# Optimization experiments

Hardware: AMD Instinct MI355X
Metric: run time of the kernel (lower is better)

Reference implementation:

```python
import jax, jax.numpy as jnp
import numpy as np

B, N, K, D, H, L = 2, 2048, 256, 768, 150, 11
REL_PROP = 2
NB = 10  # distance buckets


def _lin(key, din, dout):
    return jax.random.normal(key, (din, dout), dtype=jnp.float32) / np.sqrt(din)


def setup_inputs() -> dict:
    key = jax.random.key(0)
    ks = jax.random.split(key, 16)
    rng = np.random.default_rng(0)
    prune_idx = jnp.asarray(np.stack([np.sort(rng.permutation(N)[:K]) for _ in range(B)]), dtype=jnp.int32)
    span_begin = jnp.sort(jax.random.randint(ks[2], (B, K), 0, N - 16), axis=-1).astype(jnp.int32)
    span_end = (span_begin + jax.random.randint(ks[3], (B, K), 1, 16)).astype(jnp.int32)
    return {
        "all_span_vecs": jax.random.normal(ks[0], (B, N, D), dtype=jnp.float32),
        "update": jax.random.normal(ks[1], (B, K, D), dtype=jnp.float32),
        "square_mask": jnp.ones((B, K, K), dtype=jnp.float32),
        "span_lengths": jnp.full((B,), float(K), dtype=jnp.float32),
        "span_begin": span_begin,
        "span_end": span_end,
        "prune_indices": prune_idx,
        "w_left": _lin(ks[4], D, H), "b_left": jnp.zeros((H,), jnp.float32),
        "w_right": _lin(ks[5], D, H), "b_right": jnp.zeros((H,), jnp.float32),
        "dist_emb": jax.random.normal(ks[6], (NB, H), dtype=jnp.float32) * 0.02,
        "w_h": _lin(ks[7], H, H), "b_h": jnp.zeros((H,), jnp.float32),
        "w_out": _lin(ks[8], H, L), "b_out": jnp.zeros((L,), jnp.float32),
        "a_w": _lin(ks[9], L, D),
        "gate_w": _lin(ks[10], 2 * D, D), "gate_b": jnp.zeros((D,), jnp.float32),
        "pr_w": _lin(ks[11], D, 1), "pr_b": jnp.zeros((1,), jnp.float32),
    }


def _pair_scores(u, bins, w_left, b_left, w_right, b_right, dist_emb, w_h, b_h, w_out, b_out):
    # OptFFpairs: left/right span projections + pairwise distance embedding -> FF -> L labels
    left = u @ w_left + b_left          # [B,K,H]
    right = u @ w_right + b_right       # [B,K,H]
    h = jax.nn.relu(left[:, :, None, :] + right[:, None, :, :] + dist_emb[bins])  # [B,K,K,H]
    h = jax.nn.relu(h @ w_h + b_h)
    return h @ w_out + b_out            # [B,K,K,L]


def _add_unary(rel, ss):
    # relation_add_scores: add per-span pruner scores along both pair axes; ss: [B,K,1]
    return rel + ss[:, :, None, :] + ss[:, None, :, :]


def reference(all_span_vecs, update, square_mask, span_lengths, span_begin, span_end,
              prune_indices, w_left, b_left, w_right, b_right, dist_emb, w_h, b_h,
              w_out, b_out, a_w, gate_w, gate_b, pr_w, pr_b):
    bins = jnp.clip(jnp.abs(span_begin[:, None, :] - span_begin[:, :, None]), 0, NB - 1)  # [B,K,K]
    rel = _pair_scores(update, bins, w_left, b_left, w_right, b_right, dist_emb, w_h, b_h, w_out, b_out)
    rel = _add_unary(rel, update @ pr_w + pr_b)
    for _ in range(REL_PROP):
        probs = jax.nn.relu(rel) * square_mask[..., None]     # [B,K,K,L]
        msg = probs @ a_w                                     # A(probs): [B,K,K,D]
        # ctxt[b,j,d] = sum_i msg[b,i,j,d] * update[b,i,d] / span_lengths[b]
        ctxt = (msg * update[:, :, None, :]).sum(-3) / span_lengths[:, None, None]
        g = jax.nn.sigmoid(jnp.concatenate([update, ctxt], axis=-1) @ gate_w + gate_b)
        update = g * update + (1.0 - g) * ctxt                # MyGate
        rel = _pair_scores(update, bins, w_left, b_left, w_right, b_right, dist_emb, w_h, b_h, w_out, b_out)
        rel = _add_unary(rel, update @ pr_w + pr_b)           # pruner.scorer(update)
    # overwrite_spans: scatter updated filtered spans back into the full span tensor
    valid = jnp.arange(K)[None, :] < span_lengths[:, None]    # [B,K]
    bidx = jnp.arange(B)[:, None]
    orig = all_span_vecs[bidx, prune_indices]                 # [B,K,D]
    vals = jnp.where(valid[..., None], update, orig)
    update_all = all_span_vecs.at[bidx, prune_indices].set(vals)
    return update_all, update, rel
```

## Files before the change

kernel.cpp:

```cpp
#include <hip/hip_runtime.h>
#include <hip/hip_bf16.h>
#include <math.h>

#define BB 2
#define NN 2048
#define KK 256
#define DD 768
#define HH 150
#define LL 11
#define NBINS 10

#define KP 160
#define WP 40
#define GWP 136
#define BPAD 264

typedef __attribute__((ext_vector_type(8))) short short8;
typedef __attribute__((ext_vector_type(4))) short s16x4;
typedef __attribute__((ext_vector_type(4))) float f32x4;

#define AS_GLOBAL const __attribute__((address_space(1))) void*
#define AS_LDS __attribute__((address_space(3))) void*

__device__ inline unsigned bf2u(float lo, float hi) {
  union { __hip_bfloat162 b; unsigned u; } cv;
  cv.b = __float22bfloat162_rn(make_float2(lo, hi));
  return cv.u;
}
__device__ inline short bf1(float x) {
  union { __hip_bfloat16 b; short s; } cv;
  cv.b = __float2bfloat16(x);
  return cv.s;
}
__device__ inline float ubf(short b) {
  return __uint_as_float(((unsigned)(unsigned short)b) << 16);
}

#define PRE_PREP 110
#define PRE_CVT  192
#define PRE_TRGW 1152
#define PRE_TRWLR 240
#define PRE_TRUPD 384
#define PRE_NB (PRE_PREP + PRE_CVT + PRE_TRGW + PRE_TRWLR + PRE_TRUPD)

__global__ __launch_bounds__(256) void k_pre(
    const float* __restrict__ w_h, const float* __restrict__ w_out,
    short* __restrict__ wt, short* __restrict__ wo,
    const float* __restrict__ upd_in, short* __restrict__ updbf,
    const float* __restrict__ gate_w, short* __restrict__ gwt,
    const float* __restrict__ w_left, const float* __restrict__ w_right,
    short* __restrict__ wlrt, short* __restrict__ updT)
{
  __shared__ float tile[32][33];
  int bid = blockIdx.x;
  int t = threadIdx.x;

  if (bid < PRE_PREP) {
    int idx = bid * 256 + t;
    if (idx < KP * KP) {
      int n = idx / KP, k = idx - n * KP;
      float v = (n < HH && k < HH) ? w_h[k * HH + n] : 0.f;
      wt[idx] = bf1(v);
    }
    int idx2 = idx - KP * KP;
    if (idx2 >= 0 && idx2 < 16 * KP) {
      int n = idx2 / KP, k = idx2 - n * KP;
      float v = (n < LL && k < HH) ? w_out[k * LL + n] : 0.f;
      wo[idx2] = bf1(v);
    }
    return;
  }
  bid -= PRE_PREP;
  if (bid < PRE_CVT) {
    int idx = (bid * 256 + t) * 8;
    const float4* s4 = (const float4*)(upd_in + idx);
    float4 a = s4[0], c = s4[1];
    int4 pk;
    pk.x = (int)bf2u(a.x, a.y);
    pk.y = (int)bf2u(a.z, a.w);
    pk.z = (int)bf2u(c.x, c.y);
    pk.w = (int)bf2u(c.z, c.w);
    *(int4*)(updbf + idx) = pk;
    return;
  }
  bid -= PRE_CVT;
  if (bid < PRE_TRGW) {
    int kt = bid % 48, nt = bid / 48;
    int m0 = kt * 32, n0 = nt * 32;
    int tx = t & 31, ty = t >> 5;
    #pragma unroll
    for (int r = 0; r < 4; ++r)
      tile[ty + r * 8][tx] = gate_w[(size_t)(m0 + ty + r * 8) * DD + n0 + tx];
    __syncthreads();
    #pragma unroll
    for (int r = 0; r < 4; ++r)
      gwt[(size_t)(n0 + ty + r * 8) * (2 * DD) + m0 + tx] = bf1(tile[tx][ty + r * 8]);
    return;
  }
  bid -= PRE_TRGW;
  if (bid < PRE_TRWLR) {
    int kt = bid % 24, nt = bid / 24;
    int k0 = kt * 32, n0 = nt * 32;
    const float* src = (n0 >= KP) ? w_right : w_left;
    int col0 = n0 - (n0 >= KP ? KP : 0);
    int tx = t & 31, ty = t >> 5;
    #pragma unroll
    for (int r = 0; r < 4; ++r) {
      int col = col0 + tx;
      tile[ty + r * 8][tx] = (col < HH) ? src[(size_t)(k0 + ty + r * 8) * HH + col] : 0.f;
    }
    __syncthreads();
    #pragma unroll
    for (int r = 0; r < 4; ++r)
      wlrt[(size_t)(n0 + ty + r * 8) * DD + k0 + tx] = bf1(tile[tx][ty + r * 8]);
    return;
  }
  bid -= PRE_TRWLR;
  {
    int b = bid / 192;
    int r = bid - b * 192;
    int it = r & 7, dt = r >> 3;
    int i0 = it * 32, d0 = dt * 32;
    int tx = t & 31, ty = t >> 5;
    #pragma unroll
    for (int rr = 0; rr < 4; ++rr)
      tile[ty + rr * 8][tx] = upd_in[(size_t)(b * KK + i0 + ty + rr * 8) * DD + d0 + tx];
    __syncthreads();
    #pragma unroll
    for (int rr = 0; rr < 4; ++rr)
      updT[(size_t)(b * DD + d0 + ty + rr * 8) * KK + i0 + tx] = bf1(tile[tx][ty + rr * 8]);
  }
}

__global__ __launch_bounds__(256) void k_projss(
    const short* __restrict__ updbf, const short* __restrict__ wlrt,
    const float* __restrict__ b_left, const float* __restrict__ b_right,
    const float* __restrict__ updf, const float* __restrict__ pr_w,
    const float* __restrict__ pr_b,
    float* __restrict__ left, float* __restrict__ right, float* __restrict__ ssv)
{
  __shared__ short As[64][WP];
  __shared__ short Bs[KP][WP];
  int bidx = blockIdx.x;
  int t = threadIdx.x;

  if (bidx >= 16) {
    int row = (bidx - 16) * 4 + (t >> 6);
    int l = t & 63;
    float s = 0.f;
    for (int d = l; d < DD; d += 64) s = fmaf(updf[(size_t)row * DD + d], pr_w[d], s);
    #pragma unroll
    for (int off = 32; off > 0; off >>= 1) s += __shfl_down(s, off);
    if (l == 0) ssv[row] = s + pr_b[0];
    return;
  }

  int rbk = bidx >> 1, half = bidx & 1;
  int row0 = rbk * 64;
  const short* wsrc = wlrt + (size_t)half * KP * DD;
  int l = t & 63, w = t >> 6, lr = l & 15, lg = l >> 4;
  int ar = t >> 2, ac = t & 3;
  int i1 = t + 256, i2 = t + 512;
  f32x4 acc[10];
  #pragma unroll
  for (int nt = 0; nt < 10; ++nt) acc[nt] = (f32x4){0.f, 0.f, 0.f, 0.f};

  short8 pa, pb0, pb1, pb2 = {};
  pa  = *(const short8*)(updbf + (size_t)(row0 + ar) * DD + ac * 8);
  pb0 = *(const short8*)(wsrc + (size_t)(t >> 2) * DD + (t & 3) * 8);
  pb1 = *(const short8*)(wsrc + (size_t)(i1 >> 2) * DD + (i1 & 3) * 8);
  if (i2 < 640) pb2 = *(const short8*)(wsrc + (size_t)(i2 >> 2) * DD + (i2 & 3) * 8);

  for (int ks = 0; ks < 24; ++ks) {
    __syncthreads();
    *(short8*)&As[ar][ac * 8] = pa;
    *(short8*)&Bs[t >> 2][(t & 3) * 8] = pb0;
    *(short8*)&Bs[i1 >> 2][(i1 & 3) * 8] = pb1;
    if (i2 < 640) *(short8*)&Bs[i2 >> 2][(i2 & 3) * 8] = pb2;
    __syncthreads();
    if (ks + 1 < 24) {
      int k0 = (ks + 1) * 32;
      pa  = *(const short8*)(updbf + (size_t)(row0 + ar) * DD + k0 + ac * 8);
      pb0 = *(const short8*)(wsrc + (size_t)(t >> 2) * DD + k0 + (t & 3) * 8);
      pb1 = *(const short8*)(wsrc + (size_t)(i1 >> 2) * DD + k0 + (i1 & 3) * 8);
      if (i2 < 640) pb2 = *(const short8*)(wsrc + (size_t)(i2 >> 2) * DD + k0 + (i2 & 3) * 8);
    }
    short8 a = *(short8*)&As[w * 16 + lr][lg * 8];
    #pragma unroll
    for (int nt = 0; nt < 10; ++nt) {
      short8 b = *(short8*)&Bs[nt * 16 + lr][lg * 8];
      acc[nt] = __builtin_amdgcn_mfma_f32_16x16x32_bf16(a, b, acc[nt], 0, 0, 0);
    }
  }
  const float* bias = half ? b_right : b_left;
  float* dst = half ? right : left;
  int rowb = row0 + w * 16 + lg * 4;
  #pragma unroll
  for (int nt = 0; nt < 10; ++nt) {
    int col = nt * 16 + lr;
    if (col < HH) {
      float bv = bias[col];
      #pragma unroll
      for (int q = 0; q < 4; ++q)
        dst[(size_t)(rowb + q) * HH + col] = acc[nt][q] + bv;
    }
  }
}

template <bool WPT>
__global__ __launch_bounds__(256, 4) void k_pair_mfma(
    const float* __restrict__ left, const float* __restrict__ right,
    const float* __restrict__ ss, const int* __restrict__ span_begin,
    const float* __restrict__ demb,
    const short* __restrict__ wt, const short* __restrict__ wo,
    const float* __restrict__ b_h, const float* __restrict__ b_out,
    const float* __restrict__ mask,
    float* __restrict__ rel, short* __restrict__ probsT)
{
  int bid = blockIdx.x;
  int b  = bid >> 10;
  int r2 = bid & 1023;
  int i  = r2 >> 2;
  int j0 = (r2 & 3) * 64;

  __shared__ short wtbuf[2][32 * KP];
  __shared__ float ld_s[NBINS][KP];
  __shared__ float bh_s[KP];
  __shared__ float ssj_s[64];
  __shared__ float m_s[64];
  __shared__ int   bins[64];

  int t = threadIdx.x;
  int l = t & 63, w = t >> 6;
  int lr = l & 15, lg = l >> 4;

  auto dma_wt = [&](int s) {
    const short* src = wt + s * 5120;
    short* dst = &wtbuf[s & 1][0];
    #pragma unroll
    for (int c = 0; c < 3; ++c) {
      int idx = t + c * 256;
      if (idx < 640)
        __builtin_amdgcn_global_load_lds((AS_GLOBAL)(src + idx * 8),
                                         (AS_LDS)(dst + idx * 8), 16, 0, 0);
    }
  };

  dma_wt(0);
  int sbi = span_begin[b * KK + i];
  if (t < 64) {
    int d = span_begin[b * KK + j0 + t] - sbi; d = d < 0 ? -d : d;
    bins[t] = d > NBINS - 1 ? NBINS - 1 : d;
    ssj_s[t] = ss[b * KK + j0 + t];
    if (WPT) m_s[t] = mask[((size_t)(b * KK + i)) * KK + j0 + t];
  }
  for (int idx = t; idx < KP; idx += 256) bh_s[idx] = (idx < HH) ? b_h[idx] : 0.f;
  {
    const float* lrow = left + (size_t)(b * KK + i) * HH;
    for (int idx = t; idx < NBINS * KP; idx += 256) {
      int bn = idx / KP, k = idx - bn * KP;
      ld_s[bn][k] = (k < HH) ? (lrow[k] + demb[bn * HH + k]) : 0.f;
    }
  }
  short8 wo_f[5];
  #pragma unroll
  for (int ks = 0; ks < 5; ++ks)
    wo_f[ks] = *(const short8*)(wo + lr * KP + ks * 32 + lg * 8);

  __syncthreads();

  int jr = w * 16 + lr;
  int binr = bins[jr];
  const float* rrow = right + (size_t)(b * KK + j0 + jr) * HH;
  const float* ldr = &ld_s[binr][0];
  short8 afr[5];
  #pragma unroll
  for (int ks = 0; ks < 5; ++ks) {
    unsigned pk[4];
    #pragma unroll
    for (int e = 0; e < 4; ++e) {
      int k = ks * 32 + lg * 8 + e * 2;
      float2 r2v = (k < HH - 1) ? *(const float2*)(rrow + k) : make_float2(0.f, 0.f);
      float2 lv = *(const float2*)(ldr + k);
      float v0 = fmaxf(lv.x + r2v.x, 0.f);
      float v1 = fmaxf(lv.y + r2v.y, 0.f);
      pk[e] = bf2u(v0, v1);
    }
    int4 tmp; tmp.x = (int)pk[0]; tmp.y = (int)pk[1]; tmp.z = (int)pk[2]; tmp.w = (int)pk[3];
    afr[ks] = *(short8*)&tmp;
  }

  f32x4 acc[10];
  #pragma unroll
  for (int m = 0; m < 10; ++m) acc[m] = (f32x4){0.f, 0.f, 0.f, 0.f};

  #pragma unroll
  for (int s = 0; s < 5; ++s) {
    if (s > 0) __syncthreads();
    if (s + 1 < 5) dma_wt(s + 1);
    const short* bufp = &wtbuf[s & 1][0];
    #pragma unroll
    for (int ks = 0; ks < 5; ++ks) {
      short8 a = afr[ks];
      #pragma unroll
      for (int ntp = 0; ntp < 2; ++ntp) {
        short8 bf = *(const short8*)(bufp + (ntp * 16 + lr) * KP + ks * 32 + lg * 8);
        acc[s * 2 + ntp] = __builtin_amdgcn_mfma_f32_16x16x32_bf16(a, bf, acc[s * 2 + ntp], 0, 0, 0);
      }
    }
  }
  __syncthreads();

  short* h1 = &wtbuf[0][0];
  #pragma unroll
  for (int m = 0; m < 10; ++m) {
    int col = (m >> 1) * 32 + (m & 1) * 16 + lr;
    float bh = bh_s[col];
    #pragma unroll
    for (int q = 0; q < 4; ++q) {
      int row = w * 16 + lg * 4 + q;
      h1[row * KP + col] = bf1(fmaxf(acc[m][q] + bh, 0.f));
    }
  }
  __syncthreads();

  f32x4 acc2 = (f32x4){0.f, 0.f, 0.f, 0.f};
  #pragma unroll
  for (int ks = 0; ks < 5; ++ks) {
    short8 a = *(const short8*)(h1 + (w * 16 + lr) * KP + ks * 32 + lg * 8);
    acc2 = __builtin_amdgcn_mfma_f32_16x16x32_bf16(a, wo_f[ks], acc2, 0, 0, 0);
  }

  float ssi = ss[b * KK + i];
  float* out_s = (float*)&ld_s[0][0];
  if (lr < LL) {
    float bo = b_out[lr];
    #pragma unroll
    for (int q = 0; q < 4; ++q) {
      int row = w * 16 + lg * 4 + q;
      out_s[row * 12 + lr] = acc2[q] + bo + ssi + ssj_s[row];
    }
  }
  __syncthreads();
  if (!WPT) {
    size_t base = ((size_t)(b * KK + i) * KK + j0) * LL;
    for (int idx = t; idx < 64 * LL; idx += 256) {
      int j = idx / LL, ll2 = idx - j * LL;
      rel[base + idx] = out_s[j * 12 + ll2];
    }
  } else {
    for (int idx = t; idx < 64 * LL; idx += 256) {
      int j = idx / LL, ll2 = idx - j * LL;
      float v = fmaxf(out_s[j * 12 + ll2], 0.f) * m_s[j];
      probsT[(((size_t)(b * LL + ll2)) * KK + j0 + j) * KK + i] = bf1(v);
    }
  }
}

__global__ __launch_bounds__(256) void k_ctxt_mfma(
    const short* __restrict__ probsT, const short* __restrict__ updT,
    const float* __restrict__ a_w, const float* __restrict__ span_len,
    short* __restrict__ ctxbf)
{
  int bidx = blockIdx.x;
  int b = bidx / 192;
  int r = bidx - b * 192;
  int jt = r / 24, dt = r - jt * 24;
  int j0 = jt * 32, d0 = dt * 32;

  __shared__ short Bs[32][BPAD];
  __shared__ short As[32][BPAD];

  int t = threadIdx.x, l = t & 63, w = t >> 6, lr = l & 15, lg = l >> 4;
  int wr = w >> 1, wc = w & 1;

  for (int s = 0; s < 4; ++s) {
    int idx = t + s * 256;
    int row = idx >> 5, c = idx & 31;
    *(short8*)&Bs[row][c * 8] =
        *(const short8*)(updT + ((size_t)(b * DD + d0 + row)) * KK + c * 8);
  }

  short8 pa[4];
  #pragma unroll
  for (int s = 0; s < 4; ++s) {
    int idx = t + s * 256;
    int row = idx >> 5, c = idx & 31;
    pa[s] = *(const short8*)(probsT + (((size_t)(b * LL + 0)) * KK + j0 + row) * KK + c * 8);
  }

  f32x4 accF = (f32x4){0.f, 0.f, 0.f, 0.f};

  for (int ll = 0; ll < LL; ++ll) {
    __syncthreads();
    #pragma unroll
    for (int s = 0; s < 4; ++s) {
      int idx = t + s * 256;
      int row = idx >> 5, c = idx & 31;
      *(short8*)&As[row][c * 8] = pa[s];
    }
    if (ll + 1 < LL) {
      #pragma unroll
      for (int s = 0; s < 4; ++s) {
        int idx = t + s * 256;
        int row = idx >> 5, c = idx & 31;
        pa[s] = *(const short8*)(probsT + (((size_t)(b * LL + ll + 1)) * KK + j0 + row) * KK + c * 8);
      }
    }
    float awl = a_w[ll * DD + d0 + wc * 16 + lr];
    __syncthreads();

    f32x4 accL = (f32x4){0.f, 0.f, 0.f, 0.f};
    #pragma unroll
    for (int ks = 0; ks < 8; ++ks) {
      short8 a = *(short8*)&As[wr * 16 + lr][ks * 32 + lg * 8];
      short8 bf = *(short8*)&Bs[wc * 16 + lr][ks * 32 + lg * 8];
      accL = __builtin_amdgcn_mfma_f32_16x16x32_bf16(a, bf, accL, 0, 0, 0);
    }
    #pragma unroll
    for (int q = 0; q < 4; ++q)
      accF[q] = fmaf(awl, accL[q], accF[q]);
  }

  float inv = 1.f / span_len[b];
  int rowb = j0 + wr * 16 + lg * 4;
  int col = d0 + wc * 16 + lr;
  #pragma unroll
  for (int q = 0; q < 4; ++q) {
    size_t off = (size_t)(b * KK + rowb + q) * DD + col;
    ctxbf[off] = bf1(accF[q] * inv);
  }
}

template <bool LAST>
__global__ __launch_bounds__(256) void k_gate_mfma(
    const short* __restrict__ updbf, const short* __restrict__ ctxbf,
    const short* __restrict__ gwt, const float* __restrict__ gate_b,
    const float* __restrict__ updr, float* __restrict__ updw,
    short* __restrict__ nxtbf, short* __restrict__ updT,
    const int* __restrict__ prune, const float* __restrict__ span_len,
    float* __restrict__ out_all)
{
  int rb = blockIdx.x / 12, cb = blockIdx.x - rb * 12;
  int row0 = rb * 32, col0 = cb * 64;
  __shared__ short As[32][GWP];
  __shared__ short Bs[64][GWP];
  int t = threadIdx.x, l = t & 63, w = t >> 6, lr = l & 15, lg = l >> 4;
  int wr = w >> 1, wc = w & 1;

  f32x4 acc[2];
  acc[0] = (f32x4){0.f, 0.f, 0.f, 0.f};
  acc[1] = (f32x4){0.f, 0.f, 0.f, 0.f};

  short8 pa[2], pb[4];
  #pragma unroll
  for (int s = 0; s < 2; ++s) {
    int idx = t + s * 256;
    pa[s] = *(const short8*)(updbf + (size_t)(row0 + (idx >> 4)) * DD + (idx & 15) * 8);
  }
  #pragma unroll
  for (int s = 0; s < 4; ++s) {
    int idx = t + s * 256;
    pb[s] = *(const short8*)(gwt + (size_t)(col0 + (idx >> 4)) * (2 * DD) + (idx & 15) * 8);
  }

  for (int ph = 0; ph < 12; ++ph) {
    __syncthreads();
    #pragma unroll
    for (int s = 0; s < 2; ++s) {
      int idx = t + s * 256;
      *(short8*)&As[idx >> 4][(idx & 15) * 8] = pa[s];
    }
    #pragma unroll
    for (int s = 0; s < 4; ++s) {
      int idx = t + s * 256;
      *(short8*)&Bs[idx >> 4][(idx & 15) * 8] = pb[s];
    }
    if (ph + 1 < 12) {
      int k0 = (ph + 1) * 128;
      #pragma unroll
      for (int s = 0; s < 2; ++s) {
        int idx = t + s * 256;
        int ka = k0 + (idx & 15) * 8;
        const short* asrc = (ka < DD) ? (updbf + (size_t)(row0 + (idx >> 4)) * DD + ka)
                                      : (ctxbf + (size_t)(row0 + (idx >> 4)) * DD + ka - DD);
        pa[s] = *(const short8*)asrc;
      }
      #pragma unroll
      for (int s = 0; s < 4; ++s) {
        int idx = t + s * 256;
        pb[s] = *(const short8*)(gwt + (size_t)(col0 + (idx >> 4)) * (2 * DD) + k0 + (idx & 15) * 8);
      }
    }
    __syncthreads();
    #pragma unroll
    for (int ksub = 0; ksub < 4; ++ksub) {
      short8 a = *(short8*)&As[wr * 16 + lr][ksub * 32 + lg * 8];
      #pragma unroll
      for (int nt = 0; nt < 2; ++nt) {
        short8 bf = *(short8*)&Bs[wc * 32 + nt * 16 + lr][ksub * 32 + lg * 8];
        acc[nt] = __builtin_amdgcn_mfma_f32_16x16x32_bf16(a, bf, acc[nt], 0, 0, 0);
      }
    }
  }
  int rowb = row0 + wr * 16 + lg * 4;
  int bb = rowb >> 8, ii = rowb & 255;
  #pragma unroll
  for (int nt = 0; nt < 2; ++nt) {
    int col = col0 + wc * 32 + nt * 16 + lr;
    float gb = gate_b[col];
    s16x4 tw;
    #pragma unroll
    for (int q = 0; q < 4; ++q) {
      size_t off = (size_t)(rowb + q) * DD + col;
      float x = acc[nt][q] + gb;
      float g = 1.f / (1.f + expf(-x));
      float cv = ubf(ctxbf[off]);
      float o = g * updr[off] + (1.f - g) * cv;
      updw[off] = o;
      short bv = bf1(o);
      nxtbf[off] = bv;
      tw[q] = bv;
      if (LAST) {
        int iq = ii + q;
        if ((float)iq < span_len[bb]) {
          int dst = prune[bb * KK + iq];
          out_all[((size_t)(bb * NN + dst)) * DD + col] = o;
        }
      }
    }
    *(s16x4*)(updT + ((size_t)(bb * DD + col)) * KK + ii) = tw;
  }
}

extern "C" void kernel_launch(void* const* d_in, const int* in_sizes, int n_in,
                              void* d_out, int out_size, void* d_ws, size_t ws_size,
                              hipStream_t stream)
{
  (void)in_sizes; (void)n_in; (void)out_size; (void)ws_size;
  const float* all_span = (const float*)d_in[0];
  const float* upd_in   = (const float*)d_in[1];
  const float* mask     = (const float*)d_in[2];
  const float* span_len = (const float*)d_in[3];
  const int*   span_beg = (const int*)d_in[4];
  const int*   prune    = (const int*)d_in[6];
  const float* w_left   = (const float*)d_in[7];
  const float* b_left   = (const float*)d_in[8];
  const float* w_right  = (const float*)d_in[9];
  const float* b_right  = (const float*)d_in[10];
  const float* dist_emb = (const float*)d_in[11];
  const float* w_h      = (const float*)d_in[12];
  const float* b_h      = (const float*)d_in[13];
  const float* w_out    = (const float*)d_in[14];
  const float* b_out    = (const float*)d_in[15];
  const float* a_w      = (const float*)d_in[16];
  const float* gate_w   = (const float*)d_in[17];
  const float* gate_b   = (const float*)d_in[18];
  const float* pr_w     = (const float*)d_in[19];
  const float* pr_b     = (const float*)d_in[20];

  float* out_all = (float*)d_out;
  float* out_upd = out_all + (size_t)BB * NN * DD;
  float* out_rel = out_upd + (size_t)BB * KK * DD;

  float* ws     = (float*)d_ws;
  float* left   = ws;
  float* right  = left + (size_t)BB * KK * HH;
  float* ssv    = right + (size_t)BB * KK * HH + 64;
  short* wt_bf  = (short*)(ssv + (size_t)BB * KK);
  short* wo_bf  = wt_bf + KP * KP;
  short* updbf0 = wo_bf + 16 * KP;
  short* updbf1 = updbf0 + (size_t)BB * KK * DD;
  short* ctxbf  = updbf1 + (size_t)BB * KK * DD;
  short* gwt    = ctxbf + (size_t)BB * KK * DD;
  short* wlrt   = gwt + (size_t)DD * 2 * DD;
  short* probsT = wlrt + (size_t)2 * KP * DD;
  short* updT   = probsT + (size_t)BB * LL * KK * KK;

  hipMemcpyAsync(out_all, all_span, sizeof(float) * (size_t)BB * NN * DD,
                 hipMemcpyDeviceToDevice, stream);
  k_pre<<<PRE_NB, 256, 0, stream>>>(w_h, w_out, wt_bf, wo_bf, upd_in, updbf0,
                                    gate_w, gwt, w_left, w_right, wlrt, updT);

  k_projss<<<144, 256, 0, stream>>>(updbf0, wlrt, b_left, b_right, upd_in,
                                    pr_w, pr_b, left, right, ssv);
  k_pair_mfma<true><<<BB * KK * 4, 256, 0, stream>>>(
      left, right, ssv, span_beg, dist_emb, wt_bf, wo_bf, b_h, b_out, mask,
      out_rel, probsT);

  for (int p = 0; p < 2; ++p) {
    short* cur_bf = (p == 0) ? updbf0 : updbf1;
    short* nxt_bf = (p == 0) ? updbf1 : updbf0;
    const float* updr = (p == 0) ? upd_in : out_upd;
    k_ctxt_mfma<<<BB * 8 * 24, 256, 0, stream>>>(probsT, updT, a_w, span_len, ctxbf);
    if (p == 0) {
      k_gate_mfma<false><<<16 * 12, 256, 0, stream>>>(
          cur_bf, ctxbf, gwt, gate_b, updr, out_upd, nxt_bf, updT,
          prune, span_len, out_all);
    } else {
      k_gate_mfma<true><<<16 * 12, 256, 0, stream>>>(
          cur_bf, ctxbf, gwt, gate_b, updr, out_upd, nxt_bf, updT,
          prune, span_len, out_all);
    }
    k_projss<<<144, 256, 0, stream>>>(nxt_bf, wlrt, b_left, b_right, out_upd,
                                      pr_w, pr_b, left, right, ssv);
    if (p == 0) {
      k_pair_mfma<true><<<BB * KK * 4, 256, 0, stream>>>(
          left, right, ssv, span_beg, dist_emb, wt_bf, wo_bf, b_h, b_out, mask,
          out_rel, probsT);
    } else {
      k_pair_mfma<false><<<BB * KK * 4, 256, 0, stream>>>(
          left, right, ssv, span_beg, dist_emb, wt_bf, wo_bf, b_h, b_out, mask,
          out_rel, probsT);
    }
  }
}
```

Measured before the change: 190.9 us.

## Process two i rows per pair-MFMA block to reuse staged hidden weights

Each pair-scoring block now handles two i rows instead of one. The DMA'd w_h tiles, the right-row loads and the bin setup are shared across both rows, and the grid is halved. This amortises the per-block weight streaming and setup cost. In exchange it doubles the accumulator registers, lowers the occupancy hint from 4 to 3, reloads w_out and b_h from global memory per row instead of holding them in registers or LDS, and serialises the two output epilogues.

```diff
diff --git a/kernel.cpp b/kernel.cpp
--- a/kernel.cpp
+++ b/kernel.cpp
@@ -208,7 +208,7 @@
 }
 
 template <bool WPT>
-__global__ __launch_bounds__(256, 4) void k_pair_mfma(
+__global__ __launch_bounds__(256, 3) void k_pair_mfma(
     const float* __restrict__ left, const float* __restrict__ right,
     const float* __restrict__ ss, const int* __restrict__ span_begin,
     const float* __restrict__ demb,
@@ -218,17 +218,17 @@
     float* __restrict__ rel, short* __restrict__ probsT)
 {
   int bid = blockIdx.x;
-  int b  = bid >> 10;
-  int r2 = bid & 1023;
-  int i  = r2 >> 2;
+  int b  = bid >> 9;
+  int r2 = bid & 511;
+  int i0 = (r2 >> 2) * 2;
   int j0 = (r2 & 3) * 64;
 
   __shared__ short wtbuf[2][32 * KP];
-  __shared__ float ld_s[NBINS][KP];
-  __shared__ float bh_s[KP];
+  __shared__ float demb_s[NBINS][KP];
   __shared__ float ssj_s[64];
-  __shared__ float m_s[64];
-  __shared__ int   bins[64];
+  __shared__ float m_s[2][64];
+  __shared__ int   bins0[64];
+  __shared__ int   bins1[64];
 
   int t = threadIdx.x;
   int l = t & 63, w = t >> 6;
@@ -247,52 +247,62 @@
   };
 
   dma_wt(0);
-  int sbi = span_begin[b * KK + i];
+  int sb0 = span_begin[b * KK + i0];
+  int sb1 = span_begin[b * KK + i0 + 1];
   if (t < 64) {
-    int d = span_begin[b * KK + j0 + t] - sbi; d = d < 0 ? -d : d;
-    bins[t] = d > NBINS - 1 ? NBINS - 1 : d;
+    int sbj = span_begin[b * KK + j0 + t];
+    int d0 = sbj - sb0; d0 = d0 < 0 ? -d0 : d0;
+    int d1 = sbj - sb1; d1 = d1 < 0 ? -d1 : d1;
+    bins0[t] = d0 > NBINS - 1 ? NBINS - 1 : d0;
+    bins1[t] = d1 > NBINS - 1 ? NBINS - 1 : d1;
     ssj_s[t] = ss[b * KK + j0 + t];
-    if (WPT) m_s[t] = mask[((size_t)(b * KK + i)) * KK + j0 + t];
-  }
-  for (int idx = t; idx < KP; idx += 256) bh_s[idx] = (idx < HH) ? b_h[idx] : 0.f;
-  {
-    const float* lrow = left + (size_t)(b * KK + i) * HH;
-    for (int idx = t; idx < NBINS * KP; idx += 256) {
-      int bn = idx / KP, k = idx - bn * KP;
-      ld_s[bn][k] = (k < HH) ? (lrow[k] + demb[bn * HH + k]) : 0.f;
-    }
-  }
-  short8 wo_f[5];
-  #pragma unroll
-  for (int ks = 0; ks < 5; ++ks)
-    wo_f[ks] = *(const short8*)(wo + lr * KP + ks * 32 + lg * 8);
-
+    if (WPT) {
+      m_s[0][t] = mask[((size_t)(b * KK + i0)) * KK + j0 + t];
+      m_s[1][t] = mask[((size_t)(b * KK + i0 + 1)) * KK + j0 + t];
+    }
+  }
+  for (int idx = t; idx < NBINS * KP; idx += 256) {
+    int bn = idx / KP, k = idx - bn * KP;
+    demb_s[bn][k] = (k < HH) ? demb[bn * HH + k] : 0.f;
+  }
   __syncthreads();
 
   int jr = w * 16 + lr;
-  int binr = bins[jr];
-  const float* rrow = right + (size_t)(b * KK + j0 + jr) * HH;
-  const float* ldr = &ld_s[binr][0];
-  short8 afr[5];
+  int bin0 = bins0[jr], bin1 = bins1[jr];
+  const float* rrow  = right + (size_t)(b * KK + j0 + jr) * HH;
+  const float* lrow0 = left + (size_t)(b * KK + i0) * HH;
+  const float* lrow1 = lrow0 + HH;
+  short8 afr0[5], afr1[5];
   #pragma unroll
   for (int ks = 0; ks < 5; ++ks) {
-    unsigned pk[4];
+    unsigned pk0[4], pk1[4];
     #pragma unroll
     for (int e = 0; e < 4; ++e) {
       int k = ks * 32 + lg * 8 + e * 2;
-      float2 r2v = (k < HH - 1) ? *(const float2*)(rrow + k) : make_float2(0.f, 0.f);
-      float2 lv = *(const float2*)(ldr + k);
-      float v0 = fmaxf(lv.x + r2v.x, 0.f);
-      float v1 = fmaxf(lv.y + r2v.y, 0.f);
-      pk[e] = bf2u(v0, v1);
-    }
-    int4 tmp; tmp.x = (int)pk[0]; tmp.y = (int)pk[1]; tmp.z = (int)pk[2]; tmp.w = (int)pk[3];
-    afr[ks] = *(short8*)&tmp;
-  }
-
-  f32x4 acc[10];
-  #pragma unroll
-  for (int m = 0; m < 10; ++m) acc[m] = (f32x4){0.f, 0.f, 0.f, 0.f};
+      if (k < HH - 1) {
+        float2 rv = *(const float2*)(rrow + k);
+        float2 d0 = *(const float2*)(&demb_s[bin0][k]);
+        float2 d1 = *(const float2*)(&demb_s[bin1][k]);
+        float2 l0 = *(const float2*)(lrow0 + k);
+        float2 l1 = *(const float2*)(lrow1 + k);
+        pk0[e] = bf2u(fmaxf(l0.x + d0.x + rv.x, 0.f), fmaxf(l0.y + d0.y + rv.y, 0.f));
+        pk1[e] = bf2u(fmaxf(l1.x + d1.x + rv.x, 0.f), fmaxf(l1.y + d1.y + rv.y, 0.f));
+      } else {
+        pk0[e] = 0; pk1[e] = 0;
+      }
+    }
+    int4 t0; t0.x = (int)pk0[0]; t0.y = (int)pk0[1]; t0.z = (int)pk0[2]; t0.w = (int)pk0[3];
+    int4 t1; t1.x = (int)pk1[0]; t1.y = (int)pk1[1]; t1.z = (int)pk1[2]; t1.w = (int)pk1[3];
+    afr0[ks] = *(short8*)&t0;
+    afr1[ks] = *(short8*)&t1;
+  }
+
+  f32x4 acc0[10], acc1[10];
+  #pragma unroll
+  for (int m = 0; m < 10; ++m) {
+    acc0[m] = (f32x4){0.f, 0.f, 0.f, 0.f};
+    acc1[m] = (f32x4){0.f, 0.f, 0.f, 0.f};
+  }
 
   #pragma unroll
   for (int s = 0; s < 5; ++s) {
@@ -301,58 +311,66 @@
     const short* bufp = &wtbuf[s & 1][0];
     #pragma unroll
     for (int ks = 0; ks < 5; ++ks) {
-      short8 a = afr[ks];
       #pragma unroll
       for (int ntp = 0; ntp < 2; ++ntp) {
         short8 bf = *(const short8*)(bufp + (ntp * 16 + lr) * KP + ks * 32 + lg * 8);
-        acc[s * 2 + ntp] = __builtin_amdgcn_mfma_f32_16x16x32_bf16(a, bf, acc[s * 2 + ntp], 0, 0, 0);
+        acc0[s * 2 + ntp] = __builtin_amdgcn_mfma_f32_16x16x32_bf16(afr0[ks], bf, acc0[s * 2 + ntp], 0, 0, 0);
+        acc1[s * 2 + ntp] = __builtin_amdgcn_mfma_f32_16x16x32_bf16(afr1[ks], bf, acc1[s * 2 + ntp], 0, 0, 0);
       }
     }
   }
   __syncthreads();
 
   short* h1 = &wtbuf[0][0];
-  #pragma unroll
-  for (int m = 0; m < 10; ++m) {
-    int col = (m >> 1) * 32 + (m & 1) * 16 + lr;
-    float bh = bh_s[col];
-    #pragma unroll
-    for (int q = 0; q < 4; ++q) {
-      int row = w * 16 + lg * 4 + q;
-      h1[row * KP + col] = bf1(fmaxf(acc[m][q] + bh, 0.f));
-    }
-  }
-  __syncthreads();
-
-  f32x4 acc2 = (f32x4){0.f, 0.f, 0.f, 0.f};
-  #pragma unroll
-  for (int ks = 0; ks < 5; ++ks) {
-    short8 a = *(const short8*)(h1 + (w * 16 + lr) * KP + ks * 32 + lg * 8);
-    acc2 = __builtin_amdgcn_mfma_f32_16x16x32_bf16(a, wo_f[ks], acc2, 0, 0, 0);
-  }
-
-  float ssi = ss[b * KK + i];
-  float* out_s = (float*)&ld_s[0][0];
-  if (lr < LL) {
-    float bo = b_out[lr];
-    #pragma unroll
-    for (int q = 0; q < 4; ++q) {
-      int row = w * 16 + lg * 4 + q;
-      out_s[row * 12 + lr] = acc2[q] + bo + ssi + ssj_s[row];
-    }
-  }
-  __syncthreads();
-  if (!WPT) {
-    size_t base = ((size_t)(b * KK + i) * KK + j0) * LL;
-    for (int idx = t; idx < 64 * LL; idx += 256) {
-      int j = idx / LL, ll2 = idx - j * LL;
-      rel[base + idx] = out_s[j * 12 + ll2];
-    }
-  } else {
-    for (int idx = t; idx < 64 * LL; idx += 256) {
-      int j = idx / LL, ll2 = idx - j * LL;
-      float v = fmaxf(out_s[j * 12 + ll2], 0.f) * m_s[j];
-      probsT[(((size_t)(b * LL + ll2)) * KK + j0 + j) * KK + i] = bf1(v);
+  float* out_s = (float*)&demb_s[0][0];
+
+  #pragma unroll
+  for (int ii = 0; ii < 2; ++ii) {
+    if (ii > 0) __syncthreads();
+
+    #pragma unroll
+    for (int m = 0; m < 10; ++m) {
+      int col = (m >> 1) * 32 + (m & 1) * 16 + lr;
+      float bh = (col < HH) ? b_h[col] : 0.f;
+      f32x4 av = (ii == 0) ? acc0[m] : acc1[m];
+      #pragma unroll
+      for (int q = 0; q < 4; ++q) {
+        int row = w * 16 + lg * 4 + q;
+        h1[row * KP + col] = bf1(fmaxf(av[q] + bh, 0.f));
+      }
+    }
+    __syncthreads();
+
+    f32x4 acc2 = (f32x4){0.f, 0.f, 0.f, 0.f};
+    #pragma unroll
+    for (int ks = 0; ks < 5; ++ks) {
+      short8 a = *(const short8*)(h1 + (w * 16 + lr) * KP + ks * 32 + lg * 8);
+      short8 bfw = *(const short8*)(wo + lr * KP + ks * 32 + lg * 8);
+      acc2 = __builtin_amdgcn_mfma_f32_16x16x32_bf16(a, bfw, acc2, 0, 0, 0);
+    }
+
+    float ssi = ss[b * KK + i0 + ii];
+    if (lr < LL) {
+      float bo = b_out[lr];
+      #pragma unroll
+      for (int q = 0; q < 4; ++q) {
+        int row = w * 16 + lg * 4 + q;
+        out_s[row * 12 + lr] = acc2[q] + bo + ssi + ssj_s[row];
+      }
+    }
+    __syncthreads();
+    if (!WPT) {
+      size_t base = ((size_t)(b * KK + i0 + ii) * KK + j0) * LL;
+      for (int idx = t; idx < 64 * LL; idx += 256) {
+        int j = idx / LL, ll2 = idx - j * LL;
+        rel[base + idx] = out_s[j * 12 + ll2];
+      }
+    } else {
+      for (int idx = t; idx < 64 * LL; idx += 256) {
+        int j = idx / LL, ll2 = idx - j * LL;
+        float v = fmaxf(out_s[j * 12 + ll2], 0.f) * m_s[ii][j];
+        probsT[(((size_t)(b * LL + ll2)) * KK + j0 + j) * KK + i0 + ii] = bf1(v);
+      }
     }
   }
 }
@@ -584,7 +602,7 @@
 
   k_projss<<<144, 256, 0, stream>>>(updbf0, wlrt, b_left, b_right, upd_in,
                                     pr_w, pr_b, left, right, ssv);
-  k_pair_mfma<true><<<BB * KK * 4, 256, 0, stream>>>(
+  k_pair_mfma<true><<<BB * (KK / 2) * 4, 256, 0, stream>>>(
       left, right, ssv, span_beg, dist_emb, wt_bf, wo_bf, b_h, b_out, mask,
       out_rel, probsT);
 
@@ -605,11 +623,11 @@
     k_projss<<<144, 256, 0, stream>>>(nxt_bf, wlrt, b_left, b_right, out_upd,
                                       pr_w, pr_b, left, right, ssv);
     if (p == 0) {
-      k_pair_mfma<true><<<BB * KK * 4, 256, 0, stream>>>(
+      k_pair_mfma<true><<<BB * (KK / 2) * 4, 256, 0, stream>>>(
           left, right, ssv, span_beg, dist_emb, wt_bf, wo_bf, b_h, b_out, mask,
           out_rel, probsT);
     } else {
-      k_pair_mfma<false><<<BB * KK * 4, 256, 0, stream>>>(
+      k_pair_mfma<false><<<BB * (KK / 2) * 4, 256, 0, stream>>>(
           left, right, ssv, span_beg, dist_emb, wt_bf, wo_bf, b_h, b_out, mask,
           out_rel, probsT);
     }
```

Measured after the change: 200.2 us. +4.9%, slower.

## Shrink pair-kernel LDS footprint with single-buffered weights and aliased scratch

Applied to the files above, without the earlier changes.

Replaces the double-buffered weight tile and separate bias, left-distance and output arrays with one aliased shared slab. Weight stages are now loaded synchronously with a barrier before and after each load. The h1 scratch uses a 152-element row stride, and bias and output weights are read straight from global memory instead of being staged in LDS or held in registers. The goal is lower LDS and register use so more workgroups fit per CU, at the cost of no longer overlapping weight loads with MFMA work and adding barriers.

```diff
diff --git a/kernel.cpp b/kernel.cpp
--- a/kernel.cpp
+++ b/kernel.cpp
@@ -11,6 +11,7 @@
 #define NBINS 10
 
 #define KP 160
+#define HS 152
 #define WP 40
 #define GWP 136
 #define BPAD 264
@@ -223,26 +224,28 @@
   int i  = r2 >> 2;
   int j0 = (r2 & 3) * 64;
 
-  __shared__ short wtbuf[2][32 * KP];
-  __shared__ float ld_s[NBINS][KP];
-  __shared__ float bh_s[KP];
+  __shared__ int4 smem[1217];
   __shared__ float ssj_s[64];
   __shared__ float m_s[64];
   __shared__ int   bins[64];
 
+  short* wtslab = (short*)smem;
+  float* ld_s   = (float*)((char*)smem + 10240);
+  short* h1     = (short*)smem;
+  float* out_s  = (float*)smem;
+
   int t = threadIdx.x;
   int l = t & 63, w = t >> 6;
   int lr = l & 15, lg = l >> 4;
 
   auto dma_wt = [&](int s) {
     const short* src = wt + s * 5120;
-    short* dst = &wtbuf[s & 1][0];
     #pragma unroll
     for (int c = 0; c < 3; ++c) {
       int idx = t + c * 256;
       if (idx < 640)
         __builtin_amdgcn_global_load_lds((AS_GLOBAL)(src + idx * 8),
-                                         (AS_LDS)(dst + idx * 8), 16, 0, 0);
+                                         (AS_LDS)(wtslab + idx * 8), 16, 0, 0);
     }
   };
 
@@ -254,25 +257,19 @@
     ssj_s[t] = ss[b * KK + j0 + t];
     if (WPT) m_s[t] = mask[((size_t)(b * KK + i)) * KK + j0 + t];
   }
-  for (int idx = t; idx < KP; idx += 256) bh_s[idx] = (idx < HH) ? b_h[idx] : 0.f;
   {
     const float* lrow = left + (size_t)(b * KK + i) * HH;
     for (int idx = t; idx < NBINS * KP; idx += 256) {
       int bn = idx / KP, k = idx - bn * KP;
-      ld_s[bn][k] = (k < HH) ? (lrow[k] + demb[bn * HH + k]) : 0.f;
-    }
-  }
-  short8 wo_f[5];
-  #pragma unroll
-  for (int ks = 0; ks < 5; ++ks)
-    wo_f[ks] = *(const short8*)(wo + lr * KP + ks * 32 + lg * 8);
-
+      ld_s[bn * KP + k] = (k < HH) ? (lrow[k] + demb[bn * HH + k]) : 0.f;
+    }
+  }
   __syncthreads();
 
   int jr = w * 16 + lr;
   int binr = bins[jr];
   const float* rrow = right + (size_t)(b * KK + j0 + jr) * HH;
-  const float* ldr = &ld_s[binr][0];
+  const float* ldr = ld_s + binr * KP;
   short8 afr[5];
   #pragma unroll
   for (int ks = 0; ks < 5; ++ks) {
@@ -296,30 +293,33 @@
 
   #pragma unroll
   for (int s = 0; s < 5; ++s) {
-    if (s > 0) __syncthreads();
-    if (s + 1 < 5) dma_wt(s + 1);
-    const short* bufp = &wtbuf[s & 1][0];
+    if (s > 0) {
+      __syncthreads();
+      dma_wt(s);
+      __syncthreads();
+    }
     #pragma unroll
     for (int ks = 0; ks < 5; ++ks) {
       short8 a = afr[ks];
       #pragma unroll
       for (int ntp = 0; ntp < 2; ++ntp) {
-        short8 bf = *(const short8*)(bufp + (ntp * 16 + lr) * KP + ks * 32 + lg * 8);
+        short8 bf = *(const short8*)(wtslab + (ntp * 16 + lr) * KP + ks * 32 + lg * 8);
         acc[s * 2 + ntp] = __builtin_amdgcn_mfma_f32_16x16x32_bf16(a, bf, acc[s * 2 + ntp], 0, 0, 0);
       }
     }
   }
   __syncthreads();
 
-  short* h1 = &wtbuf[0][0];
   #pragma unroll
   for (int m = 0; m < 10; ++m) {
     int col = (m >> 1) * 32 + (m & 1) * 16 + lr;
-    float bh = bh_s[col];
-    #pragma unroll
-    for (int q = 0; q < 4; ++q) {
-      int row = w * 16 + lg * 4 + q;
-      h1[row * KP + col] = bf1(fmaxf(acc[m][q] + bh, 0.f));
+    float bh = (col < HH) ? b_h[col] : 0.f;
+    if (m < 9 || lr < 8) {
+      #pragma unroll
+      for (int q = 0; q < 4; ++q) {
+        int row = w * 16 + lg * 4 + q;
+        h1[row * HS + col] = bf1(fmaxf(acc[m][q] + bh, 0.f));
+      }
     }
   }
   __syncthreads();
@@ -327,12 +327,13 @@
   f32x4 acc2 = (f32x4){0.f, 0.f, 0.f, 0.f};
   #pragma unroll
   for (int ks = 0; ks < 5; ++ks) {
-    short8 a = *(const short8*)(h1 + (w * 16 + lr) * KP + ks * 32 + lg * 8);
-    acc2 = __builtin_amdgcn_mfma_f32_16x16x32_bf16(a, wo_f[ks], acc2, 0, 0, 0);
-  }
+    short8 a = *(const short8*)(h1 + (w * 16 + lr) * HS + ks * 32 + lg * 8);
+    short8 bfw = *(const short8*)(wo + lr * KP + ks * 32 + lg * 8);
+    acc2 = __builtin_amdgcn_mfma_f32_16x16x32_bf16(a, bfw, acc2, 0, 0, 0);
+  }
+  __syncthreads();
 
   float ssi = ss[b * KK + i];
-  float* out_s = (float*)&ld_s[0][0];
   if (lr < LL) {
     float bo = b_out[lr];
     #pragma unroll
```

Measured after the change: 186.5 us. -2.3%, faster.
